# Kernel optimization log

Measured on AMD Instinct MI355X. Metric: run time of the kernel, lower is better.

The kernel has to match this reference:

```python
import jax, jax.numpy as jnp
import numpy as np

P_DIMS = [512, 256, 128]
K_DIMS = [256, 256, 256]
NT = 65536


def setup_inputs() -> dict:
    key = jax.random.key(0)
    ks = jax.random.split(key, 8 * len(P_DIMS))
    inp = {}
    ki = 0
    for i, (p, k) in enumerate(zip(P_DIMS, K_DIMS)):
        inp[f"x{i}"] = jax.random.normal(ks[ki], (NT, p), jnp.float32); ki += 1
        inp[f"alpha{i}"] = jax.random.normal(ks[ki], (1, k), jnp.float32); ki += 1
        inp[f"beta{i}"] = jax.random.normal(ks[ki], (k, p), jnp.float32) * 0.05; ki += 1
        inp[f"sig{i}"] = jax.random.normal(ks[ki], (1, k), jnp.float32); ki += 1
        inp[f"eta{i}"] = jax.random.normal(ks[ki], (1, k), jnp.float32); ki += 1
        inp[f"gam{i}"] = jax.random.normal(ks[ki], (k, 1), jnp.float32) * 0.03; ki += 1
        inp[f"w{i}"] = jax.random.normal(ks[ki], (k, p), jnp.float32); ki += 1
        inp[f"disc{i}"] = jnp.array([3.0], jnp.float32); ki += 1
    return inp


def _source(x, alpha, beta, sig, eta, gam, w, disc):
    # x: (nt,p); w,beta: (k,p); alpha,sig,eta: (1,k); gam: (k,1); disc: (1,)
    h = eta ** 2                                           # (1,k)
    d2 = (jnp.sum(x * x, axis=1, keepdims=True)
          - 2.0 * (x @ w.T)
          + jnp.sum(w * w, axis=1)[None, :])
    a = jnp.exp(-(gam[:, 0] ** 2)[None, :] * d2)           # (nt,k)
    ah = a * h                                             # a * H
    hx = jnp.sum(ah, axis=1)                               # (nt,)
    mu = x @ beta.T + alpha                                # (nt,k)
    mux = jnp.sum(mu * ah, axis=1) / hx
    sig2x = jnp.sum((sig ** 2) * (ah ** 2), axis=1) / (hx * hx)
    hx_dc = hx * jax.nn.sigmoid(disc[0])
    return mux, sig2x, hx, hx_dc


def reference(x0, alpha0, beta0, sig0, eta0, gam0, w0, disc0,
              x1, alpha1, beta1, sig1, eta1, gam1, w1, disc1,
              x2, alpha2, beta2, sig2, eta2, gam2, w2, disc2):
    srcs = [
        (x0, alpha0, beta0, sig0, eta0, gam0, w0, disc0),
        (x1, alpha1, beta1, sig1, eta1, gam1, w1, disc1),
        (x2, alpha2, beta2, sig2, eta2, gam2, w2, disc2),
    ]
    outs = [_source(*s) for s in srcs]  # fixed small loop over sources
    mux_t = jnp.stack([o[0] for o in outs])     # (S,nt)
    sig2x_t = jnp.stack([o[1] for o in outs])
    hx_t = jnp.stack([o[2] for o in outs])
    hx_dc = jnp.stack([o[3] for o in outs])
    denom = jnp.sum(hx_dc, axis=0)
    mux_comb = jnp.sum(mux_t * hx_dc, axis=0) / denom
    sig2x_comb = jnp.sum(sig2x_t * hx_dc ** 2, axis=0) / (denom ** 2)
    mux_final = jnp.concatenate([mux_t, mux_comb[None]], axis=0)      # (S+1,nt)
    sig2x_final = jnp.concatenate([sig2x_t, sig2x_comb[None]], axis=0)
    hx_final = jnp.concatenate([hx_t, denom[None]], axis=0)
    return (mux_final, sig2x_final, hx_final)
```

## Files before the change

kernel.cpp:

```cpp
#include <hip/hip_runtime.h>
#include <hip/hip_bf16.h>

typedef __attribute__((ext_vector_type(8))) short short8;
typedef __attribute__((ext_vector_type(4))) float f32x4;

#define NT 65536

__device__ __forceinline__ unsigned short f2bf(float f) {
    union { float f; unsigned int u; } v; v.f = f;
    unsigned int u = v.u;
    unsigned int r = (u + 0x7fffu + ((u >> 16) & 1u)) >> 16;
    return (unsigned short)r;
}

__device__ __forceinline__ unsigned int cvt_pk_bf16(float lo, float hi) {
    unsigned int r;
    asm("v_cvt_pk_bf16_f32 %0, %1, %2" : "=v"(r) : "v"(lo), "v"(hi));
    return r;
}

__global__ void prep_kernel(const float* __restrict__ w0, const float* __restrict__ b0,
                            const float* __restrict__ a0, const float* __restrict__ s0,
                            const float* __restrict__ e0, const float* __restrict__ g0,
                            const float* __restrict__ w1, const float* __restrict__ b1,
                            const float* __restrict__ a1, const float* __restrict__ s1,
                            const float* __restrict__ e1, const float* __restrict__ g1,
                            const float* __restrict__ w2, const float* __restrict__ b2,
                            const float* __restrict__ a2, const float* __restrict__ s2,
                            const float* __restrict__ e2, const float* __restrict__ g2,
                            unsigned short* __restrict__ bc, float* __restrict__ prmAll) {
    __shared__ float red[2];
    const int bx = blockIdx.x;
    const int s = bx >> 9;
    const int n = bx & 511;
    const int P = 512 >> s;
    const float* w   = (s == 0) ? w0 : ((s == 1) ? w1 : w2);
    const float* bet = (s == 0) ? b0 : ((s == 1) ? b1 : b2);
    const float* alp = (s == 0) ? a0 : ((s == 1) ? a1 : a2);
    const float* sig = (s == 0) ? s0 : ((s == 1) ? s1 : s2);
    const float* eta = (s == 0) ? e0 : ((s == 1) ? e1 : e2);
    const float* gam = (s == 0) ? g0 : ((s == 1) ? g1 : g2);
    unsigned short* dstb = bc + ((s == 0) ? 0 : ((s == 1) ? (512 * 512) : (512 * 512 + 512 * 256)));
    float* prm = prmAll + 1280 * s;

    const int tid = threadIdx.x;
    const int k16 = n >> 5;
    const int typ = (n >> 4) & 1;
    const int k = k16 * 16 + (n & 15);
    const bool isw = (typ == 0);
    const float* src = (isw ? w : bet) + (size_t)k * P;
    unsigned short* dst = dstb + (size_t)n * P;
    float ss = 0.f;
    for (int c = tid; c < P; c += 128) {
        float f = src[c];
        dst[c] = f2bf(f);
        if (isw) ss += f * f;
    }
#pragma unroll
    for (int m = 1; m < 64; m <<= 1) ss += __shfl_xor(ss, m);
    if ((tid & 63) == 0) red[tid >> 6] = ss;
    __syncthreads();
    if (isw && tid == 0) prm[k] = red[0] + red[1];
    if (n == 0) {
        for (int kk = tid; kk < 256; kk += 128) {
            float g = gam[kk], e = eta[kk];
            prm[256 + kk]  = g * g;
            prm[512 + kk]  = e * e;
            prm[768 + kk]  = alp[kk];
            prm[1024 + kk] = sig[kk] * sig[kk];
        }
    }
}

template<int P>
__device__ __forceinline__ void body(const float* __restrict__ x,
                                     const unsigned short* __restrict__ Bc,
                                     const float* __restrict__ prm,
                                     float* __restrict__ pws, int h, int rg,
                                     unsigned short* AsU, float (*xn2s)[64],
                                     float (*part)[64][3], int tid) {
    constexpr int KS  = P / 32;
    constexpr int IST = P / 64;
    constexpr int WIN = (P == 256) ? 4 : 2;

    const int lane = tid & 63, wv = tid >> 6;
    const int l15 = lane & 15, l4 = lane >> 4;
    const int k16 = h * 8 + wv;

    short8 Bf[2][KS];
#pragma unroll
    for (int st = 0; st < 2; st++)
#pragma unroll
        for (int ks = 0; ks < KS; ks++)
            Bf[st][ks] = *(const short8*)(Bc + (size_t)(k16 * 32 + st * 16 + l15) * P + ks * 32 + l4 * 8);

    const int kb = k16 * 16 + 4 * l4;
    const f32x4 wn2 = *(const f32x4*)(prm + kb);
    const f32x4 g2  = *(const f32x4*)(prm + 256 + kb);
    const f32x4 hv  = *(const f32x4*)(prm + 512 + kb);
    const f32x4 alv = *(const f32x4*)(prm + 768 + kb);
    const f32x4 s2v = *(const f32x4*)(prm + 1024 + kb);

    const int srow = tid >> 3;
    const int ssl0 = tid & 7;

    {
        const int row0 = rg * 64;
        float4 pa[IST], pb[IST];
#pragma unroll
        for (int i = 0; i < IST; i++) {
            const float* gp = x + (size_t)(row0 + srow) * P + (ssl0 + 8 * i) * 8;
            pa[i] = *(const float4*)(gp);
            pb[i] = *(const float4*)(gp + 4);
        }
        float ssacc = 0.f;
#pragma unroll
        for (int i = 0; i < IST; i++) {
            float4 a0 = pa[i], a1 = pb[i];
            ssacc += a0.x*a0.x + a0.y*a0.y + a0.z*a0.z + a0.w*a0.w
                   + a1.x*a1.x + a1.y*a1.y + a1.z*a1.z + a1.w*a1.w;
            uint4 pk = { cvt_pk_bf16(a0.x, a0.y), cvt_pk_bf16(a0.z, a0.w),
                         cvt_pk_bf16(a1.x, a1.y), cvt_pk_bf16(a1.z, a1.w) };
            const int slot = ssl0 + 8 * i;
            *(uint4*)(AsU + srow * P + ((slot ^ (srow & 7)) << 3)) = pk;
        }
        ssacc += __shfl_xor(ssacc, 1);
        ssacc += __shfl_xor(ssacc, 2);
        ssacc += __shfl_xor(ssacc, 4);
        if (ssl0 == 0) xn2s[0][srow] = ssacc;
    }
    __syncthreads();

    int buf = 0;
    for (int tt = 0; tt < 8; tt++) {
        const int tile = rg + 128 * tt;
        const int row0 = tile * 64;
        const bool more = (tt < 7);
        const int nrow0 = (tile + 128) * 64;

        f32x4 acc[2][4];
#pragma unroll
        for (int st = 0; st < 2; st++)
#pragma unroll
            for (int rf = 0; rf < 4; rf++) acc[st][rf] = (f32x4){0.f, 0.f, 0.f, 0.f};

        float4 gfa[WIN], gfb[WIN];
        float ssacc = 0.f;

#pragma unroll
        for (int ks = 0; ks < KS; ks++) {
            if (more && ks >= WIN && (ks - WIN) < IST) {
                const int i = ks - WIN;
                float4 a0 = gfa[i % WIN], a1 = gfb[i % WIN];
                ssacc += a0.x*a0.x + a0.y*a0.y + a0.z*a0.z + a0.w*a0.w
                       + a1.x*a1.x + a1.y*a1.y + a1.z*a1.z + a1.w*a1.w;
                uint4 pk = { cvt_pk_bf16(a0.x, a0.y), cvt_pk_bf16(a0.z, a0.w),
                             cvt_pk_bf16(a1.x, a1.y), cvt_pk_bf16(a1.z, a1.w) };
                const int slot = ssl0 + 8 * i;
                *(uint4*)(AsU + (buf ^ 1) * 64 * P + srow * P + ((slot ^ (srow & 7)) << 3)) = pk;
            }
            if (more && ks < IST) {
                const float* gp = x + (size_t)(nrow0 + srow) * P + (ssl0 + 8 * ks) * 8;
                gfa[ks % WIN] = *(const float4*)(gp);
                gfb[ks % WIN] = *(const float4*)(gp + 4);
            }
            short8 af[4];
#pragma unroll
            for (int rf = 0; rf < 4; rf++) {
                const int row = 16 * rf + l15;
                af[rf] = *(const short8*)(AsU + buf * 64 * P + row * P + (((ks * 4 + l4) ^ (row & 7)) << 3));
            }
#pragma unroll
            for (int rf = 0; rf < 4; rf++) {
                acc[0][rf] = __builtin_amdgcn_mfma_f32_16x16x32_bf16(Bf[0][ks], af[rf], acc[0][rf], 0, 0, 0);
                acc[1][rf] = __builtin_amdgcn_mfma_f32_16x16x32_bf16(Bf[1][ks], af[rf], acc[1][rf], 0, 0, 0);
            }
        }

        if (more) {
#pragma unroll
            for (int i = (KS - WIN < 0 ? 0 : KS - WIN); i < IST; i++) {
                float4 a0 = gfa[i % WIN], a1 = gfb[i % WIN];
                ssacc += a0.x*a0.x + a0.y*a0.y + a0.z*a0.z + a0.w*a0.w
                       + a1.x*a1.x + a1.y*a1.y + a1.z*a1.z + a1.w*a1.w;
                uint4 pk = { cvt_pk_bf16(a0.x, a0.y), cvt_pk_bf16(a0.z, a0.w),
                             cvt_pk_bf16(a1.x, a1.y), cvt_pk_bf16(a1.z, a1.w) };
                const int slot = ssl0 + 8 * i;
                *(uint4*)(AsU + (buf ^ 1) * 64 * P + srow * P + ((slot ^ (srow & 7)) << 3)) = pk;
            }
            ssacc += __shfl_xor(ssacc, 1);
            ssacc += __shfl_xor(ssacc, 2);
            ssacc += __shfl_xor(ssacc, 4);
            if (ssl0 == 0) xn2s[buf ^ 1][srow] = ssacc;
        }
        __syncthreads();

#pragma unroll
        for (int rf = 0; rf < 4; rf++) {
            const int row = 16 * rf + l15;
            const float xv = xn2s[buf][row];
            float hs = 0.f, ms = 0.f, gs = 0.f;
#pragma unroll
            for (int j = 0; j < 4; j++) {
                float d2 = xv - 2.f * acc[0][rf][j] + wn2[j];
                float a  = __expf(-g2[j] * d2);
                float ah = a * hv[j];
                hs += ah;
                ms += (acc[1][rf][j] + alv[j]) * ah;
                gs += s2v[j] * ah * ah;
            }
            hs += __shfl_xor(hs, 16); hs += __shfl_xor(hs, 32);
            ms += __shfl_xor(ms, 16); ms += __shfl_xor(ms, 32);
            gs += __shfl_xor(gs, 16); gs += __shfl_xor(gs, 32);
            if (l4 == 0) { part[wv][row][0] = hs; part[wv][row][1] = ms; part[wv][row][2] = gs; }
        }
        __syncthreads();
        if (tid < 192) {
            const int v = tid >> 6, r = tid & 63;
            float sum = 0.f;
#pragma unroll
            for (int w8 = 0; w8 < 8; w8++) sum += part[w8][r][v];
            pws[(size_t)(h * 3 + v) * NT + row0 + r] = sum;
        }
        __syncthreads();
        buf ^= 1;
    }
}

__global__ __launch_bounds__(512, 1)
void fused_all(const float* __restrict__ x0, const float* __restrict__ x1, const float* __restrict__ x2,
               const unsigned short* __restrict__ bcAll, const float* __restrict__ prmAll,
               float* __restrict__ pws) {
    __shared__ unsigned short As[2][64 * 512];
    __shared__ float part[8][64][3];
    __shared__ float xn2s[2][64];

    const int bx = blockIdx.x;
    const int src = bx % 3;
    const int local = bx / 3;
    const int h = local & 1;
    const int rg = local >> 1;
    const int tid = threadIdx.x;

    if (src == 0)
        body<512>(x0, bcAll, prmAll, pws, h, rg, &As[0][0], xn2s, part, tid);
    else if (src == 1)
        body<256>(x1, bcAll + 512 * 512, prmAll + 1280, pws + (size_t)6 * NT,
                  h, rg, &As[0][0], xn2s, part, tid);
    else
        body<128>(x2, bcAll + 512 * 512 + 512 * 256, prmAll + 2560, pws + (size_t)12 * NT,
                  h, rg, &As[0][0], xn2s, part, tid);
}

__global__ void combine_kernel(const float* __restrict__ pws,
                               const float* __restrict__ d0, const float* __restrict__ d1,
                               const float* __restrict__ d2, float* __restrict__ out) {
    const int t = blockIdx.x * 256 + threadIdx.x;
    float mux[3], s2x[3], hx[3];
#pragma unroll
    for (int s = 0; s < 3; s++) {
        const float* b = pws + (size_t)s * 6 * NT;
        const float hh = b[t] + b[(size_t)3 * NT + t];
        const float mm = b[(size_t)1 * NT + t] + b[(size_t)4 * NT + t];
        const float gg = b[(size_t)2 * NT + t] + b[(size_t)5 * NT + t];
        mux[s] = mm / hh; s2x[s] = gg / (hh * hh); hx[s] = hh;
        out[(size_t)s * NT + t]       = mux[s];
        out[(size_t)(4 + s) * NT + t] = s2x[s];
        out[(size_t)(8 + s) * NT + t] = hh;
    }
    const float sd0 = 1.f / (1.f + __expf(-d0[0]));
    const float sd1 = 1.f / (1.f + __expf(-d1[0]));
    const float sd2 = 1.f / (1.f + __expf(-d2[0]));
    const float c0 = hx[0] * sd0, c1 = hx[1] * sd1, c2 = hx[2] * sd2;
    const float den = c0 + c1 + c2;
    const float muc = mux[0] * c0 + mux[1] * c1 + mux[2] * c2;
    const float sgc = s2x[0] * c0 * c0 + s2x[1] * c1 * c1 + s2x[2] * c2 * c2;
    out[(size_t)3 * NT + t]  = muc / den;
    out[(size_t)7 * NT + t]  = sgc / (den * den);
    out[(size_t)11 * NT + t] = den;
}

extern "C" void kernel_launch(void* const* d_in, const int* in_sizes, int n_in,
                              void* d_out, int out_size, void* d_ws, size_t ws_size,
                              hipStream_t stream) {
    const float* x0 = (const float*)d_in[0];
    const float* x1 = (const float*)d_in[8];
    const float* x2 = (const float*)d_in[16];

    unsigned short* bc = (unsigned short*)d_ws;
    float* prmAll = (float*)((char*)d_ws + 917504);
    float* pws    = (float*)((char*)d_ws + 917504 + 15360);
    float* out = (float*)d_out;

    prep_kernel<<<1536, 128, 0, stream>>>(
        (const float*)d_in[6],  (const float*)d_in[2],  (const float*)d_in[1],
        (const float*)d_in[3],  (const float*)d_in[4],  (const float*)d_in[5],
        (const float*)d_in[14], (const float*)d_in[10], (const float*)d_in[9],
        (const float*)d_in[11], (const float*)d_in[12], (const float*)d_in[13],
        (const float*)d_in[22], (const float*)d_in[18], (const float*)d_in[17],
        (const float*)d_in[19], (const float*)d_in[20], (const float*)d_in[21],
        bc, prmAll);

    fused_all<<<768, 512, 0, stream>>>(x0, x1, x2, bc, prmAll, pws);
    combine_kernel<<<256, 256, 0, stream>>>(pws, (const float*)d_in[7], (const float*)d_in[15],
                                            (const float*)d_in[23], out);
}
```

Before: 145.2 us.

## Split fused multi-source kernel into per-source templated launches

Replaces the single fused kernel, which dispatched on block index to one of three source bodies, with three separate templated kernel launches, one per source. Each launch sizes its shared memory to its own P, so the smaller sources no longer reserve the 64KB buffer, and each kernel's register allocation is specialised. WIN for P=512 is also raised from 2 to 4 to prefetch deeper. In exchange, the three sources now run back-to-back with 256 blocks each (fewer blocks than CUs) instead of interleaving inside one grid, which risks tail underutilisation and extra launch gaps.

```diff
diff --git a/kernel.cpp b/kernel.cpp
--- a/kernel.cpp
+++ b/kernel.cpp
@@ -73,17 +73,21 @@
 }
 
 template<int P>
-__device__ __forceinline__ void body(const float* __restrict__ x,
-                                     const unsigned short* __restrict__ Bc,
-                                     const float* __restrict__ prm,
-                                     float* __restrict__ pws, int h, int rg,
-                                     unsigned short* AsU, float (*xn2s)[64],
-                                     float (*part)[64][3], int tid) {
+__global__ __launch_bounds__(512, 1)
+void fused_src(const float* __restrict__ x, const unsigned short* __restrict__ Bc,
+               const float* __restrict__ prm, float* __restrict__ pws) {
     constexpr int KS  = P / 32;
     constexpr int IST = P / 64;
-    constexpr int WIN = (P == 256) ? 4 : 2;
-
-    const int lane = tid & 63, wv = tid >> 6;
+    constexpr int WIN = (P == 128) ? 2 : 4;
+
+    __shared__ unsigned short As[2][64 * P];
+    __shared__ float xn2s[2][64];
+    __shared__ float part[8][64][3];
+
+    const int bx = blockIdx.x;
+    const int h  = bx & 1;
+    const int rg = bx >> 1;
+    const int tid = threadIdx.x, lane = tid & 63, wv = tid >> 6;
     const int l15 = lane & 15, l4 = lane >> 4;
     const int k16 = h * 8 + wv;
 
@@ -122,7 +126,7 @@
             uint4 pk = { cvt_pk_bf16(a0.x, a0.y), cvt_pk_bf16(a0.z, a0.w),
                          cvt_pk_bf16(a1.x, a1.y), cvt_pk_bf16(a1.z, a1.w) };
             const int slot = ssl0 + 8 * i;
-            *(uint4*)(AsU + srow * P + ((slot ^ (srow & 7)) << 3)) = pk;
+            *(uint4*)(&As[0][srow * P + ((slot ^ (srow & 7)) << 3)]) = pk;
         }
         ssacc += __shfl_xor(ssacc, 1);
         ssacc += __shfl_xor(ssacc, 2);
@@ -157,7 +161,7 @@
                 uint4 pk = { cvt_pk_bf16(a0.x, a0.y), cvt_pk_bf16(a0.z, a0.w),
                              cvt_pk_bf16(a1.x, a1.y), cvt_pk_bf16(a1.z, a1.w) };
                 const int slot = ssl0 + 8 * i;
-                *(uint4*)(AsU + (buf ^ 1) * 64 * P + srow * P + ((slot ^ (srow & 7)) << 3)) = pk;
+                *(uint4*)(&As[buf ^ 1][srow * P + ((slot ^ (srow & 7)) << 3)]) = pk;
             }
             if (more && ks < IST) {
                 const float* gp = x + (size_t)(nrow0 + srow) * P + (ssl0 + 8 * ks) * 8;
@@ -168,7 +172,7 @@
 #pragma unroll
             for (int rf = 0; rf < 4; rf++) {
                 const int row = 16 * rf + l15;
-                af[rf] = *(const short8*)(AsU + buf * 64 * P + row * P + (((ks * 4 + l4) ^ (row & 7)) << 3));
+                af[rf] = *(const short8*)(&As[buf][row * P + (((ks * 4 + l4) ^ (row & 7)) << 3)]);
             }
 #pragma unroll
             for (int rf = 0; rf < 4; rf++) {
@@ -186,7 +190,7 @@
                 uint4 pk = { cvt_pk_bf16(a0.x, a0.y), cvt_pk_bf16(a0.z, a0.w),
                              cvt_pk_bf16(a1.x, a1.y), cvt_pk_bf16(a1.z, a1.w) };
                 const int slot = ssl0 + 8 * i;
-                *(uint4*)(AsU + (buf ^ 1) * 64 * P + srow * P + ((slot ^ (srow & 7)) << 3)) = pk;
+                *(uint4*)(&As[buf ^ 1][srow * P + ((slot ^ (srow & 7)) << 3)]) = pk;
             }
             ssacc += __shfl_xor(ssacc, 1);
             ssacc += __shfl_xor(ssacc, 2);
@@ -225,31 +229,6 @@
         __syncthreads();
         buf ^= 1;
     }
-}
-
-__global__ __launch_bounds__(512, 1)
-void fused_all(const float* __restrict__ x0, const float* __restrict__ x1, const float* __restrict__ x2,
-               const unsigned short* __restrict__ bcAll, const float* __restrict__ prmAll,
-               float* __restrict__ pws) {
-    __shared__ unsigned short As[2][64 * 512];
-    __shared__ float part[8][64][3];
-    __shared__ float xn2s[2][64];
-
-    const int bx = blockIdx.x;
-    const int src = bx % 3;
-    const int local = bx / 3;
-    const int h = local & 1;
-    const int rg = local >> 1;
-    const int tid = threadIdx.x;
-
-    if (src == 0)
-        body<512>(x0, bcAll, prmAll, pws, h, rg, &As[0][0], xn2s, part, tid);
-    else if (src == 1)
-        body<256>(x1, bcAll + 512 * 512, prmAll + 1280, pws + (size_t)6 * NT,
-                  h, rg, &As[0][0], xn2s, part, tid);
-    else
-        body<128>(x2, bcAll + 512 * 512 + 512 * 256, prmAll + 2560, pws + (size_t)12 * NT,
-                  h, rg, &As[0][0], xn2s, part, tid);
 }
 
 __global__ void combine_kernel(const float* __restrict__ pws,
@@ -301,7 +280,10 @@
         (const float*)d_in[19], (const float*)d_in[20], (const float*)d_in[21],
         bc, prmAll);
 
-    fused_all<<<768, 512, 0, stream>>>(x0, x1, x2, bc, prmAll, pws);
+    const size_t bcoff1 = 512 * 512, bcoff2 = 512 * 512 + 512 * 256;
+    fused_src<512><<<256, 512, 0, stream>>>(x0, bc,          prmAll,        pws);
+    fused_src<256><<<256, 512, 0, stream>>>(x1, bc + bcoff1, prmAll + 1280, pws + (size_t)6 * NT);
+    fused_src<128><<<256, 512, 0, stream>>>(x2, bc + bcoff2, prmAll + 2560, pws + (size_t)12 * NT);
     combine_kernel<<<256, 256, 0, stream>>>(pws, (const float*)d_in[7], (const float*)d_in[15],
                                             (const float*)d_in[23], out);
 }
```

After: 152.1 us. 4.8% more time.
